# Performance work log

Hardware: AMD Instinct MI355X
Metric: run time of the kernel (lower is better)

## Reference

```python
import jax, jax.numpy as jnp
import numpy as np

IN_FEATURES = 2048
OUT_FEATURES = 2048
TOP_K = 1024


def setup_inputs() -> dict:
    key = jax.random.key(0)
    kx, kw, kb = jax.random.split(key, 3)
    bound = 1.0 / np.sqrt(IN_FEATURES)
    x = jax.random.normal(kx, (8, 2048, IN_FEATURES), dtype=jnp.float32)
    weight = jax.random.uniform(kw, (OUT_FEATURES, IN_FEATURES), dtype=jnp.float32,
                                minval=-bound, maxval=bound)
    bias = jax.random.uniform(kb, (OUT_FEATURES,), dtype=jnp.float32,
                              minval=-bound, maxval=bound)
    return {"x": x, "weight": weight, "bias": bias}


def _topk_mask(weight: jnp.ndarray, k: int) -> jnp.ndarray:
    # Per output row, keep the k largest-magnitude weights (binary mask).
    _, idx = jax.lax.top_k(jnp.abs(weight), k)            # [out, k]
    rows = jnp.arange(weight.shape[0])[:, None]            # [out, 1]
    mask = jnp.zeros_like(weight).at[rows, idx].set(1.0)   # scatter ones
    return mask


def reference(x, weight, bias):
    # y = x @ (mask * W)^T + b, mask = top-k by |W| per output feature
    mask = _topk_mask(weight, TOP_K)
    masked_weight = weight * mask                          # [out, in]
    return jnp.einsum('bsi,oi->bso', x, masked_weight) + bias
```

## Files before the change

### kernel.cpp

```cpp
#include <hip/hip_runtime.h>

typedef __attribute__((ext_vector_type(8))) short s16x8;
typedef __attribute__((ext_vector_type(4))) float f32x4;
typedef __attribute__((ext_vector_type(8))) unsigned short u16x8;

#define GLB(p) ((const __attribute__((address_space(1))) void*)(p))
#define LDS(p) ((__attribute__((address_space(3))) void*)(p))

__device__ __forceinline__ unsigned short f2bf(float f) {
  unsigned u = __float_as_uint(f);
  u += 0x7fffu + ((u >> 16) & 1u);
  return (unsigned short)(u >> 16);
}

__global__ __launch_bounds__(256) void topk_mask_kernel(
    const float* __restrict__ W, unsigned short* __restrict__ Wb) {
  __shared__ int hist[4096];
  __shared__ int scanres[2];
  __shared__ int wsum[4];
  const int tid  = threadIdx.x;
  const int lane = tid & 63;
  const int wv   = tid >> 6;
  const int row  = blockIdx.x;
  const float* wr = W + (size_t)row * 2048;

  const float4 v0 = *(const float4*)(wr + tid * 8);
  const float4 v1 = *(const float4*)(wr + tid * 8 + 4);
  float val[8] = {v0.x, v0.y, v0.z, v0.w, v1.x, v1.y, v1.z, v1.w};
  unsigned key[8];
#pragma unroll
  for (int e = 0; e < 8; ++e) key[e] = __float_as_uint(val[e]) & 0x7fffffffu;

  unsigned prefix = 0;
  int rem = 1024;

  for (int i = tid; i < 4096; i += 256) hist[i] = 0;
  __syncthreads();
#pragma unroll
  for (int e = 0; e < 8; ++e) atomicAdd(&hist[key[e] >> 20], 1);
  __syncthreads();
  if (wv == 0) {
    const int base = 4096 - (lane + 1) * 64;
    int s = 0;
    for (int b = 0; b < 64; ++b) s += hist[base + b];
    int cum = s;
#pragma unroll
    for (int off = 1; off < 64; off <<= 1) {
      int o = __shfl_up(cum, off, 64);
      if (lane >= off) cum += o;
    }
    const int cumex = cum - s;
    if (cumex < rem && rem <= cum) {
      int running = cumex;
      for (int b = 63; b >= 0; --b) {
        int h = hist[base + b];
        if (running + h >= rem) { scanres[0] = base + b; scanres[1] = rem - running; break; }
        running += h;
      }
    }
  }
  __syncthreads();
  prefix = ((unsigned)scanres[0]) << 20;
  rem = scanres[1];
  __syncthreads();

  for (int i = tid; i < 1024; i += 256) hist[i] = 0;
  __syncthreads();
#pragma unroll
  for (int e = 0; e < 8; ++e)
    if ((key[e] >> 20) == (prefix >> 20)) atomicAdd(&hist[(key[e] >> 10) & 1023], 1);
  __syncthreads();
  if (wv == 0) {
    const int base = 1024 - (lane + 1) * 16;
    int s = 0;
    for (int b = 0; b < 16; ++b) s += hist[base + b];
    int cum = s;
#pragma unroll
    for (int off = 1; off < 64; off <<= 1) {
      int o = __shfl_up(cum, off, 64);
      if (lane >= off) cum += o;
    }
    const int cumex = cum - s;
    if (cumex < rem && rem <= cum) {
      int running = cumex;
      for (int b = 15; b >= 0; --b) {
        int h = hist[base + b];
        if (running + h >= rem) { scanres[0] = base + b; scanres[1] = rem - running; break; }
        running += h;
      }
    }
  }
  __syncthreads();
  prefix |= ((unsigned)scanres[0]) << 10;
  rem = scanres[1];
  __syncthreads();

  for (int i = tid; i < 1024; i += 256) hist[i] = 0;
  __syncthreads();
#pragma unroll
  for (int e = 0; e < 8; ++e)
    if ((key[e] >> 10) == (prefix >> 10)) atomicAdd(&hist[key[e] & 1023], 1);
  __syncthreads();
  if (wv == 0) {
    const int base = 1024 - (lane + 1) * 16;
    int s = 0;
    for (int b = 0; b < 16; ++b) s += hist[base + b];
    int cum = s;
#pragma unroll
    for (int off = 1; off < 64; off <<= 1) {
      int o = __shfl_up(cum, off, 64);
      if (lane >= off) cum += o;
    }
    const int cumex = cum - s;
    if (cumex < rem && rem <= cum) {
      int running = cumex;
      for (int b = 15; b >= 0; --b) {
        int h = hist[base + b];
        if (running + h >= rem) { scanres[0] = base + b; scanres[1] = rem - running; break; }
        running += h;
      }
    }
  }
  __syncthreads();
  const unsigned T = prefix | (unsigned)scanres[0];
  rem = scanres[1];

  int eqcnt = 0;
#pragma unroll
  for (int e = 0; e < 8; ++e) eqcnt += (key[e] == T) ? 1 : 0;
  int c = eqcnt;
#pragma unroll
  for (int off = 1; off < 64; off <<= 1) {
    int o = __shfl_up(c, off, 64);
    if (lane >= off) c += o;
  }
  if (lane == 63) wsum[wv] = c;
  __syncthreads();
  int wavebase = 0;
  for (int j = 0; j < wv; ++j) wavebase += wsum[j];
  const int myex = wavebase + c - eqcnt;

  u16x8 o;
  int r = 0;
#pragma unroll
  for (int e = 0; e < 8; ++e) {
    const bool iseq = (key[e] == T);
    const bool keep = (key[e] > T) || (iseq && (myex + r) < rem);
    r += iseq ? 1 : 0;
    o[e] = keep ? f2bf(val[e]) : (unsigned short)0;
  }
  *(u16x8*)(Wb + (size_t)row * 2048 + tid * 8) = o;
}

__global__ __launch_bounds__(256) void convert_x_kernel(
    const float* __restrict__ X, unsigned short* __restrict__ Y) {
  const size_t i = ((size_t)blockIdx.x * 256 + threadIdx.x) * 8;
  const float4* xp = (const float4*)(X + i);
  const float4 a = xp[0], b = xp[1];
  u16x8 o;
  o[0] = f2bf(a.x); o[1] = f2bf(a.y); o[2] = f2bf(a.z); o[3] = f2bf(a.w);
  o[4] = f2bf(b.x); o[5] = f2bf(b.y); o[6] = f2bf(b.z); o[7] = f2bf(b.w);
  *(u16x8*)(Y + i) = o;
}

__global__ __launch_bounds__(256) void gemm_bt_kernel(
    const unsigned short* __restrict__ A,
    const unsigned short* __restrict__ B,
    const float* __restrict__ bias,
    float* __restrict__ C) {
  constexpr int K = 2048;
  constexpr int N = 2048;
  __shared__ __align__(16) unsigned short lA[128 * 32];
  __shared__ __align__(16) unsigned short lB[128 * 32];

  const int tid  = threadIdx.x;
  const int lane = tid & 63;
  const int wv   = tid >> 6;
  const int tile_n = blockIdx.x, tile_m = blockIdx.y;
  const int wm = (wv >> 1) * 64;
  const int wn = (wv & 1) * 64;

  f32x4 acc[4][4] = {};

  const int srow = lane >> 2;
  const int scol = (lane & 3) * 8;
  const unsigned short* gA0 = A + (size_t)(tile_m * 128 + wv * 16 + srow) * K + scol;
  const unsigned short* gB0 = B + (size_t)(tile_n * 128 + wv * 16 + srow) * K + scol;
  unsigned short* lA0 = &lA[(wv * 16) * 32];
  unsigned short* lA1 = &lA[(64 + wv * 16) * 32];
  unsigned short* lB0 = &lB[(wv * 16) * 32];
  unsigned short* lB1 = &lB[(64 + wv * 16) * 32];
  const size_t rstep = (size_t)64 * K;

  const int fr = lane & 15;
  const int kg = (lane >> 4) * 8;

  for (int k0 = 0; k0 < K; k0 += 32) {
    __builtin_amdgcn_global_load_lds(GLB(gA0 + k0),         LDS(lA0), 16, 0, 0);
    __builtin_amdgcn_global_load_lds(GLB(gA0 + rstep + k0), LDS(lA1), 16, 0, 0);
    __builtin_amdgcn_global_load_lds(GLB(gB0 + k0),         LDS(lB0), 16, 0, 0);
    __builtin_amdgcn_global_load_lds(GLB(gB0 + rstep + k0), LDS(lB1), 16, 0, 0);
    __syncthreads();

    s16x8 af[4], bf[4];
#pragma unroll
    for (int i = 0; i < 4; ++i)
      af[i] = *(const s16x8*)&lA[(wm + i * 16 + fr) * 32 + kg];
#pragma unroll
    for (int j = 0; j < 4; ++j)
      bf[j] = *(const s16x8*)&lB[(wn + j * 16 + fr) * 32 + kg];
#pragma unroll
    for (int i = 0; i < 4; ++i)
#pragma unroll
      for (int j = 0; j < 4; ++j)
        acc[i][j] = __builtin_amdgcn_mfma_f32_16x16x32_bf16(af[i], bf[j], acc[i][j], 0, 0, 0);
    __syncthreads();
  }

  float bv[4];
#pragma unroll
  for (int j = 0; j < 4; ++j)
    bv[j] = bias[tile_n * 128 + wn + j * 16 + (lane & 15)];

  float* Cp = C + (size_t)(tile_m * 128 + wm + (lane >> 4) * 4) * N
                + tile_n * 128 + wn + (lane & 15);
#pragma unroll
  for (int i = 0; i < 4; ++i)
#pragma unroll
    for (int j = 0; j < 4; ++j)
#pragma unroll
      for (int r = 0; r < 4; ++r)
        Cp[(size_t)(i * 16 + r) * N + j * 16] = acc[i][j][r] + bv[j];
}

extern "C" void kernel_launch(void* const* d_in, const int* in_sizes, int n_in,
                              void* d_out, int out_size, void* d_ws, size_t ws_size,
                              hipStream_t stream) {
  const float* x    = (const float*)d_in[0];
  const float* w    = (const float*)d_in[1];
  const float* bias = (const float*)d_in[2];
  float* out = (float*)d_out;

  constexpr int M = 8 * 2048;
  constexpr int N = 2048;
  constexpr int K = 2048;

  unsigned short* xb = (unsigned short*)d_ws;
  unsigned short* wb = xb + (size_t)M * K;

  topk_mask_kernel<<<N, 256, 0, stream>>>(w, wb);
  convert_x_kernel<<<((size_t)M * K) / (256 * 8), 256, 0, stream>>>(x, xb);
  gemm_bt_kernel<<<dim3(N / 128, M / 128), 256, 0, stream>>>(xb, wb, bias, out);
}
```

Before: 406.7 us.

## Fuse prep kernels, deepen GEMM K-tile to 64 with XOR-swizzled LDS and tile grouping

Merges the top-k mask kernel and the x conversion kernel into one launch, with extra blocks doing the fp32-to-bf16 cast, which removes a launch and lets the two run concurrently. The GEMM K tile grows from 32 to 64, halving the barrier count per K. It also XOR-swizzles the LDS layout to avoid bank conflicts on fragment reads and remaps blocks into 4x4 groups to improve L2 reuse. LDS use doubles per block, which may lower occupancy. The large block-index branch adds some divergence cost to the prep kernel.

```diff
diff --git a/kernel.cpp b/kernel.cpp
--- a/kernel.cpp
+++ b/kernel.cpp
@@ -13,12 +13,25 @@
   return (unsigned short)(u >> 16);
 }
 
-__global__ __launch_bounds__(256) void topk_mask_kernel(
-    const float* __restrict__ W, unsigned short* __restrict__ Wb) {
+__global__ __launch_bounds__(256) void prep_kernel(
+    const float* __restrict__ W, unsigned short* __restrict__ Wb,
+    const float* __restrict__ X, unsigned short* __restrict__ Xb) {
   __shared__ int hist[4096];
   __shared__ int scanres[2];
   __shared__ int wsum[4];
   const int tid  = threadIdx.x;
+
+  if (blockIdx.x >= 2048) {
+    const size_t i = ((size_t)(blockIdx.x - 2048) * 256 + tid) * 8;
+    const float4* xp = (const float4*)(X + i);
+    const float4 a = xp[0], b = xp[1];
+    u16x8 o;
+    o[0] = f2bf(a.x); o[1] = f2bf(a.y); o[2] = f2bf(a.z); o[3] = f2bf(a.w);
+    o[4] = f2bf(b.x); o[5] = f2bf(b.y); o[6] = f2bf(b.z); o[7] = f2bf(b.w);
+    *(u16x8*)(Xb + i) = o;
+    return;
+  }
+
   const int lane = tid & 63;
   const int wv   = tid >> 6;
   const int row  = blockIdx.x;
@@ -152,17 +165,6 @@
   *(u16x8*)(Wb + (size_t)row * 2048 + tid * 8) = o;
 }
 
-__global__ __launch_bounds__(256) void convert_x_kernel(
-    const float* __restrict__ X, unsigned short* __restrict__ Y) {
-  const size_t i = ((size_t)blockIdx.x * 256 + threadIdx.x) * 8;
-  const float4* xp = (const float4*)(X + i);
-  const float4 a = xp[0], b = xp[1];
-  u16x8 o;
-  o[0] = f2bf(a.x); o[1] = f2bf(a.y); o[2] = f2bf(a.z); o[3] = f2bf(a.w);
-  o[4] = f2bf(b.x); o[5] = f2bf(b.y); o[6] = f2bf(b.z); o[7] = f2bf(b.w);
-  *(u16x8*)(Y + i) = o;
-}
-
 __global__ __launch_bounds__(256) void gemm_bt_kernel(
     const unsigned short* __restrict__ A,
     const unsigned short* __restrict__ B,
@@ -170,50 +172,67 @@
     float* __restrict__ C) {
   constexpr int K = 2048;
   constexpr int N = 2048;
-  __shared__ __align__(16) unsigned short lA[128 * 32];
-  __shared__ __align__(16) unsigned short lB[128 * 32];
+  __shared__ __align__(16) unsigned short lA[128 * 64];
+  __shared__ __align__(16) unsigned short lB[128 * 64];
 
   const int tid  = threadIdx.x;
   const int lane = tid & 63;
   const int wv   = tid >> 6;
-  const int tile_n = blockIdx.x, tile_m = blockIdx.y;
+
+  const int lin = blockIdx.y * 16 + blockIdx.x;
+  const int st = lin >> 4, wi = lin & 15;
+  const int tile_n = (st & 3) * 4 + (wi & 3);
+  const int tile_m = (st >> 2) * 4 + (wi >> 2);
+
   const int wm = (wv >> 1) * 64;
   const int wn = (wv & 1) * 64;
 
   f32x4 acc[4][4] = {};
 
-  const int srow = lane >> 2;
-  const int scol = (lane & 3) * 8;
-  const unsigned short* gA0 = A + (size_t)(tile_m * 128 + wv * 16 + srow) * K + scol;
-  const unsigned short* gB0 = B + (size_t)(tile_n * 128 + wv * 16 + srow) * K + scol;
-  unsigned short* lA0 = &lA[(wv * 16) * 32];
-  unsigned short* lA1 = &lA[(64 + wv * 16) * 32];
-  unsigned short* lB0 = &lB[(wv * 16) * 32];
-  unsigned short* lB1 = &lB[(64 + wv * 16) * 32];
-  const size_t rstep = (size_t)64 * K;
+  const int srow = lane >> 3;
+  const int sxor = ((lane & 7) ^ srow) * 8;
+  const unsigned short* gA0 = A + (size_t)(tile_m * 128 + wv * 8 + srow) * K + sxor;
+  const unsigned short* gB0 = B + (size_t)(tile_n * 128 + wv * 8 + srow) * K + sxor;
+  const size_t rstep = (size_t)32 * K;
+  unsigned short* lAq[4];
+  unsigned short* lBq[4];
+#pragma unroll
+  for (int q = 0; q < 4; ++q) {
+    lAq[q] = &lA[(q * 32 + wv * 8) * 64];
+    lBq[q] = &lB[(q * 32 + wv * 8) * 64];
+  }
 
   const int fr = lane & 15;
-  const int kg = (lane >> 4) * 8;
-
-  for (int k0 = 0; k0 < K; k0 += 32) {
-    __builtin_amdgcn_global_load_lds(GLB(gA0 + k0),         LDS(lA0), 16, 0, 0);
-    __builtin_amdgcn_global_load_lds(GLB(gA0 + rstep + k0), LDS(lA1), 16, 0, 0);
-    __builtin_amdgcn_global_load_lds(GLB(gB0 + k0),         LDS(lB0), 16, 0, 0);
-    __builtin_amdgcn_global_load_lds(GLB(gB0 + rstep + k0), LDS(lB1), 16, 0, 0);
+  const int qw = lane >> 4;
+  const int x0 = ((qw ^ (fr & 7))) * 8;
+  const int x1 = x0 ^ 32;
+  const unsigned short* la_f = &lA[(wm + fr) * 64];
+  const unsigned short* lb_f = &lB[(wn + fr) * 64];
+
+  for (int k0 = 0; k0 < K; k0 += 64) {
+#pragma unroll
+    for (int q = 0; q < 4; ++q) {
+      __builtin_amdgcn_global_load_lds(GLB(gA0 + q * rstep + k0), LDS(lAq[q]), 16, 0, 0);
+      __builtin_amdgcn_global_load_lds(GLB(gB0 + q * rstep + k0), LDS(lBq[q]), 16, 0, 0);
+    }
     __syncthreads();
 
-    s16x8 af[4], bf[4];
-#pragma unroll
-    for (int i = 0; i < 4; ++i)
-      af[i] = *(const s16x8*)&lA[(wm + i * 16 + fr) * 32 + kg];
-#pragma unroll
-    for (int j = 0; j < 4; ++j)
-      bf[j] = *(const s16x8*)&lB[(wn + j * 16 + fr) * 32 + kg];
-#pragma unroll
-    for (int i = 0; i < 4; ++i)
+#pragma unroll
+    for (int kk = 0; kk < 2; ++kk) {
+      const int xo = kk ? x1 : x0;
+      s16x8 af[4], bf[4];
+#pragma unroll
+      for (int i = 0; i < 4; ++i)
+        af[i] = *(const s16x8*)&la_f[i * 16 * 64 + xo];
 #pragma unroll
       for (int j = 0; j < 4; ++j)
-        acc[i][j] = __builtin_amdgcn_mfma_f32_16x16x32_bf16(af[i], bf[j], acc[i][j], 0, 0, 0);
+        bf[j] = *(const s16x8*)&lb_f[j * 16 * 64 + xo];
+#pragma unroll
+      for (int i = 0; i < 4; ++i)
+#pragma unroll
+        for (int j = 0; j < 4; ++j)
+          acc[i][j] = __builtin_amdgcn_mfma_f32_16x16x32_bf16(af[i], bf[j], acc[i][j], 0, 0, 0);
+    }
     __syncthreads();
   }
 
@@ -248,7 +267,7 @@
   unsigned short* xb = (unsigned short*)d_ws;
   unsigned short* wb = xb + (size_t)M * K;
 
-  topk_mask_kernel<<<N, 256, 0, stream>>>(w, wb);
-  convert_x_kernel<<<((size_t)M * K) / (256 * 8), 256, 0, stream>>>(x, xb);
+  const int conv_blocks = ((size_t)M * K) / (256 * 8);
+  prep_kernel<<<2048 + conv_blocks, 256, 0, stream>>>(w, wb, x, xb);
   gemm_bt_kernel<<<dim3(N / 128, M / 128), 256, 0, stream>>>(xb, wb, bias, out);
 }
```

After: 377.7 us. -7.1%, faster.
